# Kernel optimization log

Measured on AMD Instinct MI355X. Metric: run time of the kernel, lower is better.

## Reference

```python
import jax, jax.numpy as jnp
import numpy as np

B, S, L, D = 16, 16, 128, 768   # batch, num_sentences, max_sentence_length, hidden_size
A, T = 8, 5                      # num_args, max_arg_length
VOCAB = 500                      # small id range so arg tokens actually match


def setup_inputs() -> dict:
    key = jax.random.key(0)
    k0, k1, k2, k3, k4, k5 = jax.random.split(key, 6)
    hidden_states = jax.random.normal(k0, (B, S, L, D), dtype=jnp.float32)
    sentence_ids = jax.random.randint(k1, (B, S, L), 0, VOCAB, dtype=jnp.int64)
    # realistic attention masks: ones on a prefix of each sentence
    lens = jax.random.randint(k2, (B, S, 1), L // 2, L + 1)
    sentence_attention_masks = (jnp.arange(L)[None, None, :] < lens).astype(jnp.int32)
    predicate_ids = jax.random.randint(k3, (B, S, A, T), 0, VOCAB, dtype=jnp.int64)
    arg0_ids = jax.random.randint(k4, (B, S, A, T), 0, VOCAB, dtype=jnp.int64)
    arg1_ids = jax.random.randint(k5, (B, S, A, T), 0, VOCAB, dtype=jnp.int64)
    return {
        "hidden_states": hidden_states,
        "sentence_ids": sentence_ids,
        "sentence_attention_masks": sentence_attention_masks,
        "predicate_ids": predicate_ids,
        "arg0_ids": arg0_ids,
        "arg1_ids": arg1_ids,
    }


def _arg_embedding(arg_ids, sentence_ids, hidden):
    # match[b,s,a,t,l] = (sentence token l equals arg token t)
    match = sentence_ids[:, :, None, None, :] == arg_ids[..., None]          # [B,S,A,T,L] bool
    counts = match.sum(-1)                                                   # [B,S,A,T]
    matchf = match.astype(hidden.dtype)
    # per-arg-token mean over matching sentence positions
    avg = jnp.einsum('bsatl,bsld->bsatd', matchf, hidden)
    avg = avg / jnp.maximum(counts, 1).astype(hidden.dtype)[..., None]       # [B,S,A,T,D]
    # torch loop overwrites per token -> keep LAST nonzero token with a match
    valid = (arg_ids != 0) & (counts > 0)                                    # [B,S,A,T]
    Tn = arg_ids.shape[-1]
    last = Tn - 1 - jnp.argmax(valid[..., ::-1].astype(jnp.int32), axis=-1)  # [B,S,A]
    gathered = jnp.take_along_axis(avg, last[..., None, None], axis=3)[..., 0, :]
    return jnp.where(valid.any(-1)[..., None], gathered, jnp.zeros((), hidden.dtype))


def reference(hidden_states, sentence_ids, sentence_attention_masks,
              predicate_ids, arg0_ids, arg1_ids):
    # mean pooling over valid tokens
    m = sentence_attention_masks.astype(hidden_states.dtype)                 # [B,S,L]
    summed = jnp.einsum('bsl,bsld->bsd', m, hidden_states)
    counts = jnp.maximum(m.sum(-1, keepdims=True), 1.0)
    sentence_embeddings_avg = summed / counts                                # [B,S,D]
    predicate_embeddings = _arg_embedding(predicate_ids, sentence_ids, hidden_states)
    arg0_embeddings = _arg_embedding(arg0_ids, sentence_ids, hidden_states)
    arg1_embeddings = _arg_embedding(arg1_ids, sentence_ids, hidden_states)
    return (sentence_embeddings_avg, predicate_embeddings, arg0_embeddings, arg1_embeddings)
```

## Files before the change

### kernel.cpp

```cpp
#include <hip/hip_runtime.h>


namespace {
constexpr int Bc = 16, Sc = 16, Lc = 128, Dc = 768, Ac = 8, Tc = 5;
constexpr int NF4   = Dc / 4;
constexpr int NSLOT = 3 * Ac;
constexpr int BLOCK = 768;
constexpr int OUT1  = Bc * Sc * NF4;
constexpr int OUTG  = Bc * Sc * Ac * NF4;
}

__global__ __launch_bounds__(BLOCK) void srl_fused(
    const float4* __restrict__ hid,
    const int*    __restrict__ sids,
    const int*    __restrict__ amask,
    const int*    __restrict__ pids,
    const int*    __restrict__ a0ids,
    const int*    __restrict__ a1ids,
    float4*       __restrict__ out)
{
  const int bs  = blockIdx.x;
  const int tid = threadIdx.x;
  const int q   = tid % NF4;
  const int r   = tid / NF4;

  __shared__ int    sid[Lc];
  __shared__ short  slist[NSLOT][Lc];
  __shared__ int    scnt[NSLOT];
  __shared__ float4 red[BLOCK];

  int mval = 0;
  if (tid < Lc) {
    sid[tid] = sids[bs * Lc + tid];
    mval     = amask[bs * Lc + tid];
  }
  const int len = __syncthreads_count(mval != 0);

  const float4* __restrict__ hrow = hid + (size_t)bs * Lc * NF4;

  if (tid < NSLOT) {
    const int g = tid / Ac, a = tid % Ac;
    const int* ids = (g == 0 ? pids : (g == 1 ? a0ids : a1ids)) + (bs * Ac + a) * Tc;
    int tok[Tc], cnt[Tc];
#pragma unroll
    for (int t = 0; t < Tc; ++t) { tok[t] = ids[t]; cnt[t] = 0; }
    for (int l = 0; l < Lc; ++l) {
      const int v = sid[l];
#pragma unroll
      for (int t = 0; t < Tc; ++t) cnt[t] += (v == tok[t]) ? 1 : 0;
    }
    int sel = 0, n = 0;
#pragma unroll
    for (int t = Tc - 1; t >= 0; --t) {
      if (n == 0 && tok[t] != 0 && cnt[t] > 0) { sel = tok[t]; n = cnt[t]; }
    }
    scnt[tid] = n;
    if (n > 0) {
      int k = 0;
      for (int l = 0; l < Lc; ++l)
        if (sid[l] == sel) slist[tid][k++] = (short)l;
    }
  }

  float ax = 0.f, ay = 0.f, az = 0.f, aw = 0.f;
  for (int l = r; l < len; l += 4) {
    const float4 v = hrow[l * NF4 + q];
    ax += v.x; ay += v.y; az += v.z; aw += v.w;
  }
  red[tid] = make_float4(ax, ay, az, aw);
  __syncthreads();

  if (tid < NF4) {
    const float4 s0 = red[q];
    const float4 s1 = red[NF4 + q];
    const float4 s2 = red[2 * NF4 + q];
    const float4 s3 = red[3 * NF4 + q];
    const float inv = 1.0f / (float)(len > 0 ? len : 1);
    float4 o;
    o.x = (s0.x + s1.x + s2.x + s3.x) * inv;
    o.y = (s0.y + s1.y + s2.y + s3.y) * inv;
    o.z = (s0.z + s1.z + s2.z + s3.z) * inv;
    o.w = (s0.w + s1.w + s2.w + s3.w) * inv;
    out[bs * NF4 + q] = o;
  }

  for (int j = r; j < NSLOT; j += 4) {
    const int n = scnt[j];
    float ox = 0.f, oy = 0.f, oz = 0.f, ow = 0.f;
    if (n > 0) {
      for (int i = 0; i < n; ++i) {
        const int l = (int)slist[j][i];
        const float4 v = hrow[l * NF4 + q];
        ox += v.x; oy += v.y; oz += v.z; ow += v.w;
      }
      const float inv = 1.0f / (float)n;
      ox *= inv; oy *= inv; oz *= inv; ow *= inv;
    }
    const int g = j / Ac, a = j % Ac;
    out[OUT1 + g * OUTG + (bs * Ac + a) * NF4 + q] = make_float4(ox, oy, oz, ow);
  }
}

extern "C" void kernel_launch(void* const* d_in, const int* in_sizes, int n_in,
                              void* d_out, int out_size, void* d_ws, size_t ws_size,
                              hipStream_t stream) {
  const float4* hid   = (const float4*)d_in[0];
  const int*    sids  = (const int*)d_in[1];
  const int*    amask = (const int*)d_in[2];
  const int*    pids  = (const int*)d_in[3];
  const int*    a0ids = (const int*)d_in[4];
  const int*    a1ids = (const int*)d_in[5];
  float4*       out   = (float4*)d_out;

  srl_fused<<<dim3(Bc * Sc), dim3(BLOCK), 0, stream>>>(
      hid, sids, amask, pids, a0ids, a1ids, out);
}
```

Before: 165.1 us.

## Split hidden dimension across blocks to raise grid parallelism

The kernel now launches a 2D grid with six D-chunks per sentence, each 256-thread block covering 32 float4 columns with 8 row-partitions instead of one 768-thread block per sentence. This raises the block count from 256 to 1536 so more CUs have work and more loads are in flight, and the pooling loop is unrolled. In exchange every block redundantly loads the sentence ids and rebuilds the per-slot match lists, and each row read is a 512-byte segment rather than a full 3 KB row.

```diff
diff --git a/kernel.cpp b/kernel.cpp
--- a/kernel.cpp
+++ b/kernel.cpp
@@ -3,11 +3,14 @@
 
 namespace {
 constexpr int Bc = 16, Sc = 16, Lc = 128, Dc = 768, Ac = 8, Tc = 5;
-constexpr int NF4   = Dc / 4;
-constexpr int NSLOT = 3 * Ac;
-constexpr int BLOCK = 768;
-constexpr int OUT1  = Bc * Sc * NF4;
-constexpr int OUTG  = Bc * Sc * Ac * NF4;
+constexpr int NF4    = Dc / 4;
+constexpr int CHUNK  = 32;
+constexpr int NCHUNK = NF4 / CHUNK;
+constexpr int BLOCK  = 256;
+constexpr int RP     = BLOCK / CHUNK;
+constexpr int NSLOT  = 3 * Ac;
+constexpr int OUT1   = Bc * Sc * NF4;
+constexpr int OUTG   = Bc * Sc * Ac * NF4;
 }
 
 __global__ __launch_bounds__(BLOCK) void srl_fused(
@@ -19,10 +22,11 @@
     const int*    __restrict__ a1ids,
     float4*       __restrict__ out)
 {
-  const int bs  = blockIdx.x;
+  const int c   = blockIdx.x;
+  const int bs  = blockIdx.y;
   const int tid = threadIdx.x;
-  const int q   = tid % NF4;
-  const int r   = tid / NF4;
+  const int q   = tid & (CHUNK - 1);
+  const int r   = tid >> 5;
 
   __shared__ int    sid[Lc];
   __shared__ short  slist[NSLOT][Lc];
@@ -36,7 +40,7 @@
   }
   const int len = __syncthreads_count(mval != 0);
 
-  const float4* __restrict__ hrow = hid + (size_t)bs * Lc * NF4;
+  const float4* __restrict__ hrow = hid + (size_t)bs * Lc * NF4 + c * CHUNK;
 
   if (tid < NSLOT) {
     const int g = tid / Ac, a = tid % Ac;
@@ -63,28 +67,27 @@
   }
 
   float ax = 0.f, ay = 0.f, az = 0.f, aw = 0.f;
-  for (int l = r; l < len; l += 4) {
+#pragma unroll 4
+  for (int l = r; l < len; l += RP) {
     const float4 v = hrow[l * NF4 + q];
     ax += v.x; ay += v.y; az += v.z; aw += v.w;
   }
   red[tid] = make_float4(ax, ay, az, aw);
   __syncthreads();
 
-  if (tid < NF4) {
-    const float4 s0 = red[q];
-    const float4 s1 = red[NF4 + q];
-    const float4 s2 = red[2 * NF4 + q];
-    const float4 s3 = red[3 * NF4 + q];
+  if (tid < CHUNK) {
+    float4 s = red[q];
+#pragma unroll
+    for (int p = 1; p < RP; ++p) {
+      const float4 t = red[p * CHUNK + q];
+      s.x += t.x; s.y += t.y; s.z += t.z; s.w += t.w;
+    }
     const float inv = 1.0f / (float)(len > 0 ? len : 1);
-    float4 o;
-    o.x = (s0.x + s1.x + s2.x + s3.x) * inv;
-    o.y = (s0.y + s1.y + s2.y + s3.y) * inv;
-    o.z = (s0.z + s1.z + s2.z + s3.z) * inv;
-    o.w = (s0.w + s1.w + s2.w + s3.w) * inv;
-    out[bs * NF4 + q] = o;
+    s.x *= inv; s.y *= inv; s.z *= inv; s.w *= inv;
+    out[bs * NF4 + c * CHUNK + q] = s;
   }
 
-  for (int j = r; j < NSLOT; j += 4) {
+  for (int j = r; j < NSLOT; j += RP) {
     const int n = scnt[j];
     float ox = 0.f, oy = 0.f, oz = 0.f, ow = 0.f;
     if (n > 0) {
@@ -97,7 +100,8 @@
       ox *= inv; oy *= inv; oz *= inv; ow *= inv;
     }
     const int g = j / Ac, a = j % Ac;
-    out[OUT1 + g * OUTG + (bs * Ac + a) * NF4 + q] = make_float4(ox, oy, oz, ow);
+    out[OUT1 + g * OUTG + (bs * Ac + a) * NF4 + c * CHUNK + q] =
+        make_float4(ox, oy, oz, ow);
   }
 }
 
@@ -112,6 +116,6 @@
   const int*    a1ids = (const int*)d_in[5];
   float4*       out   = (float4*)d_out;
 
-  srl_fused<<<dim3(Bc * Sc), dim3(BLOCK), 0, stream>>>(
+  srl_fused<<<dim3(NCHUNK, Bc * Sc), dim3(BLOCK), 0, stream>>>(
       hid, sids, amask, pids, a0ids, a1ids, out);
 }
```

After: 159.0 us. -3.7%, faster.
